# Performance work log

Hardware: AMD Instinct MI355X
Metric: run time of the kernel (lower is better)

## Reference

```python
import jax, jax.numpy as jnp
import numpy as np

H = 16      # num_attention_heads
HD = 32     # attention_head_size
W = 7       # window size (per side)
N = W * W   # tokens per window = 49
MW = 64     # windows per image (mask_shape)
C = H * HD  # dim = 512
B = 2048    # total windows = images * MW


def _relative_position_index():
    coords = np.stack(np.meshgrid(np.arange(W), np.arange(W), indexing='ij'))  # [2,W,W]
    cf = coords.reshape(2, -1)                      # [2, N]
    rel = cf[:, :, None] - cf[:, None, :]           # [2, N, N]
    rel = rel.transpose(1, 2, 0).copy()             # [N, N, 2]
    rel[:, :, 0] += W - 1
    rel[:, :, 1] += W - 1
    rel[:, :, 0] *= 2 * W - 1
    return jnp.asarray(rel.sum(-1), dtype=jnp.int32)  # [N, N] indices into bias table

REL_IDX = _relative_position_index()


def setup_inputs() -> dict:
    key = jax.random.key(0)
    ks = jax.random.split(key, 9)
    s = 0.02
    return {
        "hidden_states": jax.random.normal(ks[0], (B, N, C), jnp.float32),
        "attention_mask": jax.random.normal(ks[1], (MW, N, N), jnp.float32),
        "wq": jax.random.normal(ks[2], (C, C), jnp.float32) * s,
        "bq": jax.random.normal(ks[3], (C,), jnp.float32) * s,
        "wk": jax.random.normal(ks[4], (C, C), jnp.float32) * s,
        "bk": jax.random.normal(ks[5], (C,), jnp.float32) * s,
        "wv": jax.random.normal(ks[6], (C, C), jnp.float32) * s,
        "bv": jax.random.normal(ks[7], (C,), jnp.float32) * s,
        "bias_table": jax.random.normal(ks[8], ((2 * W - 1) ** 2, H), jnp.float32) * s,
    }


def reference(hidden_states, attention_mask, wq, bq, wk, bk, wv, bv, bias_table):
    # hidden_states: [B, N, C]
    def proj(w, b):
        y = hidden_states @ w.T + b                  # [B, N, C]
        return y.reshape(B, N, H, HD).transpose(0, 2, 1, 3)  # [B, H, N, HD]

    q = proj(wq, bq)
    k = proj(wk, bk)
    v = proj(wv, bv)

    inv_sqrt_d = 1.0 / jnp.sqrt(jnp.float32(HD))
    scores = jnp.einsum('bhnd,bhmd->bhnm', q, k) * inv_sqrt_d  # [B, H, N, N]

    # relative position bias gather: [N, N, H] -> [H, N, N]
    rel_bias = bias_table[REL_IDX].transpose(2, 0, 1)
    scores = scores + rel_bias[None]

    # shifted-window mask: broadcast over image groups and heads
    scores = scores.reshape(B // MW, MW, H, N, N) + attention_mask[None, :, None]
    scores = scores.reshape(B, H, N, N)

    probs = jax.nn.softmax(scores, axis=-1)
    ctx = jnp.einsum('bhnm,bhmd->bhnd', probs, v)    # [B, H, N, HD]
    return ctx.transpose(0, 2, 1, 3).reshape(B, N, C)
```

## Files before the change

### kernel.cpp

```cpp
#include <hip/hip_runtime.h>
#include <hip/hip_bf16.h>
#include <string.h>

typedef unsigned short u16;
typedef __attribute__((ext_vector_type(8))) short short8;
typedef __attribute__((ext_vector_type(4))) float floatx4;
typedef __attribute__((ext_vector_type(4))) unsigned short ushort4v;
typedef __attribute__((ext_vector_type(8))) unsigned short ushort8v;
typedef __attribute__((ext_vector_type(2))) unsigned int uint2v;

#define NWIN 2048
#define NTOK 49
#define NH 16
#define HDIM 32
#define CDIM 512
#define MTOT (NWIN * NTOK)
#define NOUT (3 * CDIM)
#define KDIM CDIM

__device__ inline float b2f(u16 u) {
    unsigned int x = ((unsigned int)u) << 16;
    float f; __builtin_memcpy(&f, &x, 4); return f;
}
__device__ inline u16 f2b(float f) {
    unsigned int u; __builtin_memcpy(&u, &f, 4);
    unsigned int r = (u + 0x7fffu + ((u >> 16) & 1u)) >> 16;
    return (u16)r;
}
__device__ inline void gload16(const void* g, void* l) {
    __builtin_amdgcn_global_load_lds((const __attribute__((address_space(1))) unsigned int*)g,
                                     (__attribute__((address_space(3))) unsigned int*)l, 16, 0, 0);
}

__global__ void k_cvt_x(const float4* __restrict__ x, ushort4v* __restrict__ xb, int n4) {
    int i = blockIdx.x * blockDim.x + threadIdx.x;
    int stride = gridDim.x * blockDim.x;
    for (; i < n4; i += stride) {
        float4 v = x[i];
        ushort4v o = { f2b(v.x), f2b(v.y), f2b(v.z), f2b(v.w) };
        xb[i] = o;
    }
}

__global__ void k_pack_w(const float* __restrict__ wq, const float* __restrict__ wk,
                         const float* __restrict__ wv, const float* __restrict__ bq,
                         const float* __restrict__ bk, const float* __restrict__ bv,
                         u16* __restrict__ wout, float* __restrict__ bout) {
    const int WN = CDIM * CDIM;
    int i = blockIdx.x * blockDim.x + threadIdx.x;
    if (i < 3 * WN) {
        const float* src = (i < WN) ? wq : (i < 2 * WN ? wk : wv);
        wout[i] = f2b(src[i & (WN - 1)]);
    }
    if (i < 3 * CDIM) {
        const float* sb = (i < CDIM) ? bq : (i < 2 * CDIM ? bk : bv);
        bout[i] = sb[i & (CDIM - 1)];
    }
}

__global__ void k_bm(const float* __restrict__ mask, const float* __restrict__ bt,
                     float* __restrict__ bm) {
    int t = blockIdx.x;
    int w = t >> 4, h = t & 15;
    for (int e = threadIdx.x; e < NTOK * NTOK; e += blockDim.x) {
        int j = e / 49, i = e - j * 49;
        int ri = i / 7, ci = i - ri * 7;
        int rj = j / 7, cj = j - rj * 7;
        int idx = (ri - rj + 6) * 13 + (ci - cj + 6);
        bm[(size_t)t * 2401 + e] = bt[idx * 16 + h] + mask[(size_t)w * 2401 + i * 49 + j];
    }
}

__global__ __launch_bounds__(256)
void k_gemm(const u16* __restrict__ A, const u16* __restrict__ Bw,
            const float* __restrict__ bias, u16* __restrict__ C) {
    __shared__ __align__(16) u16 As[128 * 32];
    __shared__ __align__(16) u16 Bs[128 * 32];
    const int tid = threadIdx.x;
    const int lane = tid & 63;
    const int wave = tid >> 6;
    const int n0 = blockIdx.x * 128;
    const int m0 = blockIdx.y * 128;
    const int mh = (wave & 1) * 64;
    const int nh = (wave >> 1) * 64;

    floatx4 acc[4][4];
#pragma unroll
    for (int mi = 0; mi < 4; mi++)
#pragma unroll
        for (int ni = 0; ni < 4; ni++)
            acc[mi][ni] = (floatx4){0.f, 0.f, 0.f, 0.f};

    const int rA1 = tid >> 2, c1 = tid & 3;
    const int rA2 = rA1 + 64;
    const int cg1 = c1 ^ ((rA1 >> 1) & 3);
    const int cg2 = c1 ^ ((rA2 >> 1) & 3);
    const u16* pa1 = A + (size_t)(m0 + rA1) * KDIM + cg1 * 8;
    const u16* pa2 = A + (size_t)(m0 + rA2) * KDIM + cg2 * 8;
    const u16* pb1 = Bw + (size_t)(n0 + rA1) * KDIM + cg1 * 8;
    const u16* pb2 = Bw + (size_t)(n0 + rA2) * KDIM + cg2 * 8;
    u16* la1 = &As[tid * 8];
    u16* la2 = &As[(tid + 256) * 8];
    u16* lb1 = &Bs[tid * 8];
    u16* lb2 = &Bs[(tid + 256) * 8];

    int aoff[4], boff[4];
    const int quad = lane >> 4;
#pragma unroll
    for (int mi = 0; mi < 4; mi++) {
        int r = mh + mi * 16 + (lane & 15);
        aoff[mi] = r * 32 + (quad ^ ((r >> 1) & 3)) * 8;
        int rn = nh + mi * 16 + (lane & 15);
        boff[mi] = rn * 32 + (quad ^ ((rn >> 1) & 3)) * 8;
    }

    for (int ks = 0; ks < 16; ++ks) {
        const int k0 = ks * 32;
        gload16(pa1 + k0, la1);
        gload16(pa2 + k0, la2);
        gload16(pb1 + k0, lb1);
        gload16(pb2 + k0, lb2);
        __syncthreads();
        short8 af[4], bf[4];
#pragma unroll
        for (int mi = 0; mi < 4; mi++) af[mi] = *(const short8*)&As[aoff[mi]];
#pragma unroll
        for (int ni = 0; ni < 4; ni++) bf[ni] = *(const short8*)&Bs[boff[ni]];
#pragma unroll
        for (int mi = 0; mi < 4; mi++)
#pragma unroll
            for (int ni = 0; ni < 4; ni++)
                acc[mi][ni] = __builtin_amdgcn_mfma_f32_16x16x32_bf16(af[mi], bf[ni], acc[mi][ni], 0, 0, 0);
        __syncthreads();
    }

    const int colc = lane & 15;
#pragma unroll
    for (int ni = 0; ni < 4; ni++) {
        int gn = n0 + nh + ni * 16 + colc;
        float bv_ = bias[gn];
#pragma unroll
        for (int mi = 0; mi < 4; mi++) {
            size_t gmb = (size_t)(m0 + mh + mi * 16 + quad * 4);
#pragma unroll
            for (int r = 0; r < 4; r++)
                C[(gmb + r) * NOUT + gn] = f2b(acc[mi][ni][r] + bv_);
        }
    }
}

__global__ __launch_bounds__(256, 3)
void k_attn(const u16* __restrict__ qkv, const float* __restrict__ bmT,
            float* __restrict__ out) {
    __shared__ __align__(16) char smem[4 * 12288];
    const int lane = threadIdx.x & 63;
    const int wave = threadIdx.x >> 6;
    const int task = blockIdx.x * 4 + wave;
    const int b = task >> 4;
    const int h = task & 15;
    const int c = lane & 15;
    const int quad = lane >> 4;
    char* Vs = smem + wave * 12288;
    char* Ps = Vs + 4096;

    const u16* qbase = qkv + (size_t)b * NTOK * NOUT + h * 32;

    short8 kf[4], qf[4];
#pragma unroll
    for (int mi = 0; mi < 4; mi++) {
        int jr = mi * 16 + c; jr = jr > 48 ? 48 : jr;
        kf[mi] = *(const short8*)(qbase + (size_t)jr * NOUT + 512 + quad * 8);
    }
#pragma unroll
    for (int ni = 0; ni < 4; ni++) {
        int ir = ni * 16 + c; ir = ir > 48 ? 48 : ir;
        qf[ni] = *(const short8*)(qbase + (size_t)ir * NOUT + quad * 8);
    }

#pragma unroll
    for (int it = 0; it < 4; it++) {
        int j = it * 16 + (lane >> 2);
        int part = lane & 3;
        ushort8v val = {0, 0, 0, 0, 0, 0, 0, 0};
        if (j < 49) val = *(const ushort8v*)(qbase + (size_t)j * NOUT + 1024 + part * 8);
        int byt = (j * 64 + part * 16) ^ (((j >> 3) & 3) << 4);
        *(ushort8v*)(Vs + byt) = val;
    }

    floatx4 acc[4][4];
#pragma unroll
    for (int mi = 0; mi < 4; mi++)
#pragma unroll
        for (int ni = 0; ni < 4; ni++)
            acc[mi][ni] = (floatx4){0.f, 0.f, 0.f, 0.f};
#pragma unroll
    for (int mi = 0; mi < 4; mi++)
#pragma unroll
        for (int ni = 0; ni < 4; ni++)
            acc[mi][ni] = __builtin_amdgcn_mfma_f32_16x16x32_bf16(kf[mi], qf[ni], acc[mi][ni], 0, 0, 0);

    const float scale = 0.17677669529663687f;
    const float* bmrow = bmT + ((size_t)((b & 63) * 16 + h)) * 2401;
#pragma unroll
    for (int mi = 0; mi < 4; mi++)
#pragma unroll
        for (int r = 0; r < 4; r++) {
            int j = mi * 16 + quad * 4 + r;
            int jc = j > 48 ? 48 : j;
            const float* bp = bmrow + jc * 49;
#pragma unroll
            for (int ni = 0; ni < 4; ni++) {
                int i = ni * 16 + c;
                int ic = i > 48 ? 48 : i;
                acc[mi][ni][r] = acc[mi][ni][r] * scale + bp[ic];
            }
        }

#pragma unroll
    for (int ni = 0; ni < 4; ni++) {
        float mx = -3.0e38f;
#pragma unroll
        for (int mi = 0; mi < 3; mi++)
#pragma unroll
            for (int r = 0; r < 4; r++) mx = fmaxf(mx, acc[mi][ni][r]);
        if (quad == 0) mx = fmaxf(mx, acc[3][ni][0]);
        mx = fmaxf(mx, __shfl_xor(mx, 16));
        mx = fmaxf(mx, __shfl_xor(mx, 32));
        float sum = 0.f;
#pragma unroll
        for (int mi = 0; mi < 3; mi++)
#pragma unroll
            for (int r = 0; r < 4; r++) {
                float e = __expf(acc[mi][ni][r] - mx);
                acc[mi][ni][r] = e; sum += e;
            }
        float e0 = (quad == 0) ? __expf(acc[3][ni][0] - mx) : 0.f;
        acc[3][ni][0] = e0; sum += e0;
        acc[3][ni][1] = 0.f; acc[3][ni][2] = 0.f; acc[3][ni][3] = 0.f;
        sum += __shfl_xor(sum, 16);
        sum += __shfl_xor(sum, 32);
        float inv = 1.0f / sum;
#pragma unroll
        for (int mi = 0; mi < 4; mi++)
#pragma unroll
            for (int r = 0; r < 4; r++) acc[mi][ni][r] *= inv;
    }

    const int cx = (c & 7) << 4;
#pragma unroll
    for (int ni = 0; ni < 4; ni++) {
        char* prow = Ps + (ni * 16 + c) * 128;
#pragma unroll
        for (int mi = 0; mi < 4; mi++) {
            unsigned int d0, d1;
            asm("v_cvt_pk_bf16_f32 %0, %1, %2" : "=v"(d0) : "v"(acc[mi][ni][0]), "v"(acc[mi][ni][1]));
            asm("v_cvt_pk_bf16_f32 %0, %1, %2" : "=v"(d1) : "v"(acc[mi][ni][2]), "v"(acc[mi][ni][3]));
            uint2v w2 = { d0, d1 };
            *(uint2v*)(prow + ((mi * 32 + quad * 8) ^ cx)) = w2;
        }
    }

    asm volatile("s_waitcnt lgkmcnt(0)" ::: "memory");

    floatx4 acc2[4][2];
#pragma unroll
    for (int mi = 0; mi < 4; mi++)
#pragma unroll
        for (int ni = 0; ni < 2; ni++) acc2[mi][ni] = (floatx4){0.f, 0.f, 0.f, 0.f};
    const int vb0 = quad * 512 + (((0 * 16 + c) * 2) ^ (quad << 4));
    const int vb1 = quad * 512 + (((1 * 16 + c) * 2) ^ (quad << 4));
#pragma unroll
    for (int kk = 0; kk < 2; kk++) {
        const int plow = (kk * 64 + quad * 16) ^ cx;
        short8 pf[4];
#pragma unroll
        for (int mi = 0; mi < 4; mi++)
            pf[mi] = *(const short8*)(Ps + mi * 2048 + c * 128 + plow);
        short8 vf[2];
#pragma unroll
        for (int ni = 0; ni < 2; ni++) {
            const char* vbp = Vs + (ni ? vb1 : vb0) + kk * 2048;
#pragma unroll
            for (int z = 0; z < 8; z++)
                vf[ni][z] = *(const short*)(vbp + z * 64);
        }
#pragma unroll
        for (int mi = 0; mi < 4; mi++)
#pragma unroll
            for (int ni = 0; ni < 2; ni++)
                acc2[mi][ni] = __builtin_amdgcn_mfma_f32_16x16x32_bf16(pf[mi], vf[ni], acc2[mi][ni], 0, 0, 0);
    }

    float* ob = out + (size_t)b * 49 * CDIM + h * 32;
#pragma unroll
    for (int mi = 0; mi < 4; mi++)
#pragma unroll
        for (int r = 0; r < 4; r++) {
            int i = mi * 16 + quad * 4 + r;
            if (i < 49) {
                float* orow = ob + (size_t)i * CDIM + c;
#pragma unroll
                for (int ni = 0; ni < 2; ni++)
                    orow[ni * 16] = acc2[mi][ni][r];
            }
        }
}

extern "C" void kernel_launch(void* const* d_in, const int* in_sizes, int n_in,
                              void* d_out, int out_size, void* d_ws, size_t ws_size,
                              hipStream_t stream) {
    const float* hs   = (const float*)d_in[0];
    const float* mask = (const float*)d_in[1];
    const float* wq   = (const float*)d_in[2];
    const float* bq   = (const float*)d_in[3];
    const float* wk   = (const float*)d_in[4];
    const float* bk   = (const float*)d_in[5];
    const float* wv   = (const float*)d_in[6];
    const float* bv   = (const float*)d_in[7];
    const float* bt   = (const float*)d_in[8];
    float* out = (float*)d_out;

    char* ws = (char*)d_ws;
    size_t off = 0;
    u16* xb = (u16*)(ws + off);      off += (size_t)MTOT * CDIM * 2;
    u16* wb = (u16*)(ws + off);      off += (size_t)NOUT * KDIM * 2;
    float* biasb = (float*)(ws + off); off += (size_t)NOUT * 4;
    off = (off + 255) & ~(size_t)255;
    float* bm = (float*)(ws + off);  off += (size_t)1024 * 2401 * 4;
    off = (off + 255) & ~(size_t)255;
    u16* qkv = (u16*)(ws + off);     off += (size_t)MTOT * NOUT * 2;

    k_cvt_x<<<4096, 256, 0, stream>>>((const float4*)hs, (ushort4v*)xb, MTOT * CDIM / 4);
    k_pack_w<<<3072, 256, 0, stream>>>(wq, wk, wv, bq, bk, bv, wb, biasb);
    k_bm<<<1024, 256, 0, stream>>>(mask, bt, bm);
    k_gemm<<<dim3(12, 784), 256, 0, stream>>>(xb, wb, biasb, qkv);
    k_attn<<<8192, 256, 0, stream>>>(qkv, bm, out);
}
```

Before: 728.6 us.

## Replace QKV GEMM with 256x256 tiled double-buffered pipelined MFMA kernel

The QKV projection GEMM moves from 128x128 tiles with 4 waves to 256x256 tiles with 8 waves, 64-wide K steps and double-buffered LDS staging. Global loads for the next K-steps are interleaved with MFMA quadrants under explicit waitcnt, barriers and setprio scheduling. Workgroup indices are swizzled for L2 locality, and the epilogue writes packed bf16 outputs with vector stores. This aims to raise arithmetic intensity and hide load latency. It uses 128KB of LDS and many registers, which limits occupancy, and the hand-scheduled waitcnt counts are fragile.

```diff
diff --git a/kernel.cpp b/kernel.cpp
--- a/kernel.cpp
+++ b/kernel.cpp
@@ -71,82 +71,135 @@
     }
 }
 
-__global__ __launch_bounds__(256)
-void k_gemm(const u16* __restrict__ A, const u16* __restrict__ Bw,
-            const float* __restrict__ bias, u16* __restrict__ C) {
-    __shared__ __align__(16) u16 As[128 * 32];
-    __shared__ __align__(16) u16 Bs[128 * 32];
+__global__ __launch_bounds__(512, 2)
+void k_gemm256(const u16* __restrict__ A, const u16* __restrict__ Bw,
+               const float* __restrict__ bias, u16* __restrict__ C) {
+    __shared__ __align__(16) u16 lds[65536];
     const int tid = threadIdx.x;
     const int lane = tid & 63;
     const int wave = tid >> 6;
-    const int n0 = blockIdx.x * 128;
-    const int m0 = blockIdx.y * 128;
-    const int mh = (wave & 1) * 64;
-    const int nh = (wave >> 1) * 64;
-
-    floatx4 acc[4][4];
-#pragma unroll
-    for (int mi = 0; mi < 4; mi++)
-#pragma unroll
-        for (int ni = 0; ni < 4; ni++)
-            acc[mi][ni] = (floatx4){0.f, 0.f, 0.f, 0.f};
-
-    const int rA1 = tid >> 2, c1 = tid & 3;
-    const int rA2 = rA1 + 64;
-    const int cg1 = c1 ^ ((rA1 >> 1) & 3);
-    const int cg2 = c1 ^ ((rA2 >> 1) & 3);
-    const u16* pa1 = A + (size_t)(m0 + rA1) * KDIM + cg1 * 8;
-    const u16* pa2 = A + (size_t)(m0 + rA2) * KDIM + cg2 * 8;
-    const u16* pb1 = Bw + (size_t)(n0 + rA1) * KDIM + cg1 * 8;
-    const u16* pb2 = Bw + (size_t)(n0 + rA2) * KDIM + cg2 * 8;
-    u16* la1 = &As[tid * 8];
-    u16* la2 = &As[(tid + 256) * 8];
-    u16* lb1 = &Bs[tid * 8];
-    u16* lb2 = &Bs[(tid + 256) * 8];
-
-    int aoff[4], boff[4];
+    const int wm = wave >> 2;
+    const int wn = wave & 3;
+    const int c = lane & 15;
     const int quad = lane >> 4;
-#pragma unroll
-    for (int mi = 0; mi < 4; mi++) {
-        int r = mh + mi * 16 + (lane & 15);
-        aoff[mi] = r * 32 + (quad ^ ((r >> 1) & 3)) * 8;
-        int rn = nh + mi * 16 + (lane & 15);
-        boff[mi] = rn * 32 + (quad ^ ((rn >> 1) & 3)) * 8;
-    }
-
-    for (int ks = 0; ks < 16; ++ks) {
-        const int k0 = ks * 32;
-        gload16(pa1 + k0, la1);
-        gload16(pa2 + k0, la2);
-        gload16(pb1 + k0, lb1);
-        gload16(pb2 + k0, lb2);
-        __syncthreads();
-        short8 af[4], bf[4];
-#pragma unroll
-        for (int mi = 0; mi < 4; mi++) af[mi] = *(const short8*)&As[aoff[mi]];
-#pragma unroll
-        for (int ni = 0; ni < 4; ni++) bf[ni] = *(const short8*)&Bs[boff[ni]];
-#pragma unroll
-        for (int mi = 0; mi < 4; mi++)
-#pragma unroll
-            for (int ni = 0; ni < 4; ni++)
-                acc[mi][ni] = __builtin_amdgcn_mfma_f32_16x16x32_bf16(af[mi], bf[ni], acc[mi][ni], 0, 0, 0);
-        __syncthreads();
-    }
-
-    const int colc = lane & 15;
-#pragma unroll
-    for (int ni = 0; ni < 4; ni++) {
-        int gn = n0 + nh + ni * 16 + colc;
-        float bv_ = bias[gn];
-#pragma unroll
-        for (int mi = 0; mi < 4; mi++) {
-            size_t gmb = (size_t)(m0 + mh + mi * 16 + quad * 4);
-#pragma unroll
-            for (int r = 0; r < 4; r++)
-                C[(gmb + r) * NOUT + gn] = f2b(acc[mi][ni][r] + bv_);
-        }
-    }
+
+    const int wg = blockIdx.x;
+    const int swz = (wg & 7) * 294 + (wg >> 3);
+    const int m0 = (swz / 6) * 256;
+    const int n0 = (swz % 6) * 256;
+
+    const int r1 = tid >> 3;
+    const int cg = ((tid & 7) ^ (r1 & 7)) * 8;
+    const int bpr = (r1 & 15) * 4 + (r1 >> 4);
+    const u16* pA00 = A + (size_t)(m0 + r1) * KDIM + cg;
+    const u16* pA01 = A + (size_t)(m0 + 64 + r1) * KDIM + cg;
+    const u16* pA10 = A + (size_t)(m0 + 128 + r1) * KDIM + cg;
+    const u16* pA11 = A + (size_t)(m0 + 192 + r1) * KDIM + cg;
+    const u16* pB00 = Bw + (size_t)(n0 + bpr) * KDIM + cg;
+    const u16* pB01 = Bw + (size_t)(n0 + 64 + bpr) * KDIM + cg;
+    const u16* pB10 = Bw + (size_t)(n0 + 128 + bpr) * KDIM + cg;
+    const u16* pB11 = Bw + (size_t)(n0 + 192 + bpr) * KDIM + cg;
+
+#define STG(P0, P1, BUFU, HALFU, KOFF) \
+    gload16(P0 + (KOFF), lds + (BUFU) + (HALFU) + tid * 8); \
+    gload16(P1 + (KOFF), lds + (BUFU) + (HALFU) + 4096 + tid * 8);
+#define STG_A0(T)  STG(pA00, pA01, 0, 0, (T)*64)
+#define STG_A1(T)  STG(pA10, pA11, 0, 8192, (T)*64)
+#define STG_B0(T)  STG(pB00, pB01, 0, 16384, (T)*64)
+#define STG_B1(T)  STG(pB10, pB11, 0, 24576, (T)*64)
+#define STG_A0b(T) STG(pA00, pA01, 32768, 0, (T)*64)
+#define STG_A1b(T) STG(pA10, pA11, 32768, 8192, (T)*64)
+#define STG_B0b(T) STG(pB00, pB01, 32768, 16384, (T)*64)
+#define STG_B1b(T) STG(pB10, pB11, 32768, 24576, (T)*64)
+
+    const char* ldsc = (const char*)lds;
+    const int aBase = wm * 16384;
+    const int bBase = 32768 + (wn >> 1) * 16384 + (wn & 1) * 8192;
+    const int cx = (c & 7) << 4;
+    const int kq0 = (quad * 16) ^ cx;
+    const int kq1 = (64 + quad * 16) ^ cx;
+
+    short8 af[4][2];
+    short8 bf[2][2][2];
+    floatx4 acc[8][4];
+#pragma unroll
+    for (int mf = 0; mf < 8; mf++)
+#pragma unroll
+        for (int nf = 0; nf < 4; nf++)
+            acc[mf][nf] = (floatx4){0.f, 0.f, 0.f, 0.f};
+
+#define LDA(BUF, MH) { _Pragma("unroll") for (int mi = 0; mi < 4; mi++) { \
+        const char* pp_ = ldsc + (BUF)*65536 + aBase + (MH)*8192 + (mi*16 + c)*128; \
+        af[mi][0] = *(const short8*)(pp_ + kq0); \
+        af[mi][1] = *(const short8*)(pp_ + kq1); } }
+#define LDB(BUF, NH) { _Pragma("unroll") for (int ni = 0; ni < 2; ni++) { \
+        const char* pp_ = ldsc + (BUF)*65536 + bBase + (NH)*4096 + (ni*16 + c)*128; \
+        bf[NH][ni][0] = *(const short8*)(pp_ + kq0); \
+        bf[NH][ni][1] = *(const short8*)(pp_ + kq1); } }
+#define BAR __builtin_amdgcn_s_barrier()
+#define WAITLGKM { asm volatile("s_waitcnt lgkmcnt(0)" ::: "memory"); __builtin_amdgcn_sched_barrier(0); }
+#define MQ(MH, NH) do { __builtin_amdgcn_s_setprio(1); \
+    _Pragma("unroll") for (int kk = 0; kk < 2; kk++) \
+    _Pragma("unroll") for (int mi = 0; mi < 4; mi++) \
+    _Pragma("unroll") for (int ni = 0; ni < 2; ni++) \
+        acc[(MH)*4 + mi][(NH)*2 + ni] = __builtin_amdgcn_mfma_f32_16x16x32_bf16( \
+            af[mi][kk], bf[NH][ni][kk], acc[(MH)*4 + mi][(NH)*2 + ni], 0, 0, 0); \
+    __builtin_amdgcn_s_setprio(0); } while (0)
+
+#define GITER(T2, T3, ST, VM4) \
+     LDA(0,0); LDB(0,0);                               BAR; WAITLGKM; MQ(0,0); BAR; \
+     LDB(0,1);                                         BAR; WAITLGKM; MQ(0,1); BAR; \
+     LDA(0,1); if (ST) { STG_B0(T2); }                 BAR; WAITLGKM; MQ(1,0); BAR; \
+     if (ST) { STG_B1(T2); STG_A0(T2); }               BAR; WAITLGKM; MQ(1,1); \
+            asm volatile("s_waitcnt " VM4 ::: "memory");      BAR; \
+     LDA(1,0); LDB(1,0); if (ST) { STG_A1(T2); }       BAR; WAITLGKM; MQ(0,0); BAR; \
+     LDB(1,1);                                         BAR; WAITLGKM; MQ(0,1); BAR; \
+     LDA(1,1); if (ST) { STG_B0b(T3); }                BAR; WAITLGKM; MQ(1,0); BAR; \
+     if (ST) { STG_B1b(T3); STG_A0b(T3); STG_A1b(T3); } BAR; WAITLGKM; MQ(1,1); \
+            if (ST) { asm volatile("s_waitcnt vmcnt(8)" ::: "memory"); } BAR;
+
+    STG_A0(0); STG_A1(0); STG_B0(0); STG_B1(0);
+    STG_A0b(1); STG_A1b(1); STG_B0b(1); STG_B1b(1);
+    asm volatile("s_waitcnt vmcnt(8)" ::: "memory");
+    BAR;
+
+    GITER(2, 3, 1, "vmcnt(6)")
+    GITER(4, 5, 1, "vmcnt(6)")
+    GITER(6, 7, 1, "vmcnt(6)")
+    GITER(8, 9, 0, "vmcnt(0)")
+
+    const float4 bb = *(const float4*)&bias[n0 + wn * 64 + c * 4];
+    u16* cbase = C + (size_t)(m0 + wm * 128 + quad * 4) * NOUT + n0 + wn * 64 + c * 4;
+#pragma unroll
+    for (int mf = 0; mf < 8; mf++) {
+#pragma unroll
+        for (int r = 0; r < 4; r++) {
+            float x0 = acc[mf][0][r] + bb.x;
+            float x1 = acc[mf][1][r] + bb.y;
+            float x2 = acc[mf][2][r] + bb.z;
+            float x3 = acc[mf][3][r] + bb.w;
+            unsigned int d0, d1;
+            asm("v_cvt_pk_bf16_f32 %0, %1, %2" : "=v"(d0) : "v"(x0), "v"(x1));
+            asm("v_cvt_pk_bf16_f32 %0, %1, %2" : "=v"(d1) : "v"(x2), "v"(x3));
+            uint2v w2 = { d0, d1 };
+            *(uint2v*)(cbase + (size_t)(mf * 16 + r) * NOUT) = w2;
+        }
+    }
+#undef STG
+#undef STG_A0
+#undef STG_A1
+#undef STG_B0
+#undef STG_B1
+#undef STG_A0b
+#undef STG_A1b
+#undef STG_B0b
+#undef STG_B1b
+#undef LDA
+#undef LDB
+#undef BAR
+#undef WAITLGKM
+#undef MQ
+#undef GITER
 }
 
 __global__ __launch_bounds__(256, 3)
@@ -333,6 +386,6 @@
     k_cvt_x<<<4096, 256, 0, stream>>>((const float4*)hs, (ushort4v*)xb, MTOT * CDIM / 4);
     k_pack_w<<<3072, 256, 0, stream>>>(wq, wk, wv, bq, bk, bv, wb, biasb);
     k_bm<<<1024, 256, 0, stream>>>(mask, bt, bm);
-    k_gemm<<<dim3(12, 784), 256, 0, stream>>>(xb, wb, biasb, qkv);
+    k_gemm256<<<2352, 512, 0, stream>>>(xb, wb, biasb, qkv);
     k_attn<<<8192, 256, 0, stream>>>(qkv, bm, out);
 }
```

After: 648.1 us. 1.12x faster.
